# Optimization experiments

Hardware: AMD Instinct MI355X
Metric: run time of the kernel (lower is better)

The kernel has to match this reference:

```python
import jax, jax.numpy as jnp
import numpy as np

N_NODES = 50000
N_EDGES = 800000
EPS = 0.1

def setup_inputs() -> dict:
    key = jax.random.key(0)
    ks = jax.random.split(key, 6)
    x = jax.random.normal(ks[0], (N_NODES, 256), dtype=jnp.float32)
    edge_index = jax.random.randint(ks[1], (2, N_EDGES), 0, N_NODES, dtype=jnp.int64)
    W1 = jax.random.normal(ks[2], (256, 64), dtype=jnp.float32) * (1.0 / np.sqrt(256))
    b1 = jnp.zeros((64,), dtype=jnp.float32)
    att = jax.random.normal(ks[3], (2, 1, 64), dtype=jnp.float32) * (1.0 / np.sqrt(64))
    W2 = jax.random.normal(ks[4], (64, 16), dtype=jnp.float32) * (1.0 / np.sqrt(64))
    b2 = jnp.zeros((16,), dtype=jnp.float32)
    return {"x": x, "edge_index": edge_index, "W1": W1, "b1": b1, "att": att, "W2": W2, "b2": b2}

def _fagcn_conv(x, row, col, norm, att_l, eps):
    # message: norm * x_j gathered at source (row), scatter-add to target (col)
    msg = norm[:, None] * x[row]                      # [E_tot, H]
    x_l = jax.ops.segment_sum(msg, col, num_segments=N_NODES)  # low-pass
    x_h = -eps * x_l                                   # high-pass message = -eps * low message
    gate = jax.nn.sigmoid(jnp.sum(x * att_l, axis=-1, keepdims=True))  # [N,1]
    return gate * x_l + (1.0 - gate) * x_h

def reference(x, edge_index, W1, b1, att, W2, b2):
    # add self loops once (same edge set is reused by every layer)
    loops = jnp.arange(N_NODES, dtype=edge_index.dtype)
    row = jnp.concatenate([edge_index[0], loops])
    col = jnp.concatenate([edge_index[1], loops])
    deg = jax.ops.segment_sum(jnp.ones_like(col, dtype=x.dtype), col, num_segments=N_NODES)
    dinv = jnp.where(deg > 0, jax.lax.rsqrt(jnp.maximum(deg, 1e-30)), 0.0)
    norm = dinv[row] * dinv[col]                       # [E_tot]
    # eval mode: dropout is identity
    h = jax.nn.relu(x @ W1 + b1)                       # [N, H]
    for l in range(att.shape[0]):
        h = _fagcn_conv(h, row, col, norm, att[l], EPS)
    return h @ W2 + b2                                 # [N, out]
```

## Files before the change

### kernel.cpp

```cpp
#include <hip/hip_runtime.h>
#include <math.h>

#define N_FEAT_IN 256
#define N_HID 64
#define N_OUT 16
#define EPS 0.1f

typedef short bf16x8 __attribute__((ext_vector_type(8)));
typedef float f32x4 __attribute__((ext_vector_type(4)));

__device__ inline uint pack2(ushort a, ushort b) { return (uint)a | ((uint)b << 16); }

__device__ inline ushort bf16_rne(float x) {
    uint b = __float_as_uint(x);
    b += 0x7fff + ((b >> 16) & 1);
    return (ushort)(b >> 16);
}

__device__ inline float blo(uint u) { return __uint_as_float(u << 16); }
__device__ inline float bhi(uint u) { return __uint_as_float(u & 0xffff0000u); }

__device__ inline void split_bf16(float x, ushort& hi, ushort& lo) {
    uint b = __float_as_uint(x);
    hi = (ushort)(b >> 16);
    float xl = x - __uint_as_float(b & 0xffff0000u);
    lo = (ushort)(__float_as_uint(xl) >> 16);
}


__global__ void zero_int(int* __restrict__ p, int n) {
    int i = blockIdx.x * blockDim.x + threadIdx.x;
    if (i < n) p[i] = 0;
}


__global__ void hist_rank(const int* __restrict__ col, const int* __restrict__ row,
                          int* __restrict__ cnt, uint* __restrict__ rr, int E) {
    int e = blockIdx.x * blockDim.x + threadIdx.x;
    if (e < E) {
        int r = atomicAdd(&cnt[col[e]], 1);
        rr[e] = ((uint)r << 16) | (uint)row[e];
    }
}


__global__ void scan_chunks(const int* __restrict__ cnt, int* __restrict__ rowptr,
                            int* __restrict__ partial, float* __restrict__ dinv, int N) {
    __shared__ int sm[256];
    int tid = threadIdx.x;
    int gid = blockIdx.x * 256 + tid;
    int v = (gid < N) ? cnt[gid] : 0;
    sm[tid] = v;
    __syncthreads();
#pragma unroll
    for (int off = 1; off < 256; off <<= 1) {
        int add = (tid >= off) ? sm[tid - off] : 0;
        __syncthreads();
        sm[tid] += add;
        __syncthreads();
    }
    if (gid < N) {
        rowptr[gid] = sm[tid] - v;
        dinv[gid] = rsqrtf(1.0f + (float)v);
    }
    if (tid == 255) partial[blockIdx.x] = sm[255];
}


__global__ void scan_finish(int* __restrict__ rowptr, const int* __restrict__ partial,
                            int N, int E, int nchunks) {
    __shared__ int sm[256];
    int tid = threadIdx.x;
    sm[tid] = (tid < nchunks) ? partial[tid] : 0;
    __syncthreads();
#pragma unroll
    for (int off = 1; off < 256; off <<= 1) {
        int add = (tid >= off) ? sm[tid - off] : 0;
        __syncthreads();
        sm[tid] += add;
        __syncthreads();
    }
    int boff = (blockIdx.x == 0) ? 0 : sm[blockIdx.x - 1];
    __syncthreads();
    int gid = blockIdx.x * 256 + tid;
    if (gid < N) rowptr[gid] += boff;
    if (gid == 0) rowptr[N] = E;
}


__global__ void csr_scatter_part(const int* __restrict__ col, const uint* __restrict__ rr,
                                 const int* __restrict__ rowptr,
                                 ushort* __restrict__ srcidx, int E, int rangeSz) {
    int r = blockIdx.x & 7;
    int nsl = gridDim.x >> 3;
    int s = blockIdx.x >> 3;
    int lo = r * rangeSz;
    int hi = lo + rangeSz;
    int stride = nsl * blockDim.x;
    for (int e = s * blockDim.x + threadIdx.x; e < E; e += stride) {
        int c = col[e];
        if (c >= lo && c < hi) {
            uint v = rr[e];
            srcidx[rowptr[c] + (v >> 16)] = (ushort)(v & 0xffffu);
        }
    }
}


__global__ __launch_bounds__(256) void gemm1_mfma(const float* __restrict__ x,
                                                  const float* __restrict__ W1,
                                                  const float* __restrict__ b1,
                                                  const float* __restrict__ dinv,
                                                  uint* __restrict__ AsOut,
                                                  int MB) {
    __shared__ uint4 wh_lds[2048];
    __shared__ uint4 wl_lds[2048];
    __shared__ float4 xt4[1024];
    int tid = threadIdx.x;
    for (int e = tid; e < 2048; e += 256) {
        int ks = e >> 8;
        int rem = e & 255;
        int nt = rem >> 6;
        int ln = rem & 63;
        int k0 = ks * 32 + ((ln >> 4) << 3);
        int colw = nt * 16 + (ln & 15);
        ushort hi[8], lo[8];
#pragma unroll
        for (int i = 0; i < 8; ++i) {
            float v = W1[(k0 + i) * 64 + colw];
            split_bf16(v, hi[i], lo[i]);
        }
        wh_lds[e] = make_uint4(pack2(hi[0], hi[1]), pack2(hi[2], hi[3]),
                               pack2(hi[4], hi[5]), pack2(hi[6], hi[7]));
        wl_lds[e] = make_uint4(pack2(lo[0], lo[1]), pack2(lo[2], lo[3]),
                               pack2(lo[4], lo[5]), pack2(lo[6], lo[7]));
    }

    int lane = tid & 63;
    int m = lane & 15;
    int g = lane >> 4;
    int w = tid >> 6;
    const bf16x8* whf = reinterpret_cast<const bf16x8*>(wh_lds);
    const bf16x8* wlf = reinterpret_cast<const bf16x8*>(wl_lds);
    float bias = b1[w * 16 + m];
    int swz = m & 7;

    for (int mb = blockIdx.x; mb < MB; mb += gridDim.x) {
        __syncthreads();
        const float4* xg = reinterpret_cast<const float4*>(x) + (size_t)mb * 1024;
#pragma unroll
        for (int t = 0; t < 4; ++t) {
            int F = t * 256 + tid;
            int r = F >> 6, c4 = F & 63;
            xt4[r * 64 + (c4 ^ (r & 7))] = xg[F];
        }
        __syncthreads();

        f32x4 acc = {0.f, 0.f, 0.f, 0.f};
#pragma unroll
        for (int ks = 0; ks < 8; ++ks) {
            int c4 = ks * 8 + g * 2;
            float4 a0 = xt4[m * 64 + ((c4) ^ swz)];
            float4 a1 = xt4[m * 64 + ((c4 + 1) ^ swz)];
            float f[8] = {a0.x, a0.y, a0.z, a0.w, a1.x, a1.y, a1.z, a1.w};
            bf16x8 ah, al;
#pragma unroll
            for (int i = 0; i < 8; ++i) {
                ushort hu, lu;
                split_bf16(f[i], hu, lu);
                ah[i] = (short)hu;
                al[i] = (short)lu;
            }
            bf16x8 wh = whf[(ks * 4 + w) * 64 + lane];
            bf16x8 wl = wlf[(ks * 4 + w) * 64 + lane];
            acc = __builtin_amdgcn_mfma_f32_16x16x32_bf16(ah, wh, acc, 0, 0, 0);
            acc = __builtin_amdgcn_mfma_f32_16x16x32_bf16(al, wh, acc, 0, 0, 0);
            acc = __builtin_amdgcn_mfma_f32_16x16x32_bf16(ah, wl, acc, 0, 0, 0);
        }

        int r0 = mb * 16 + g * 4;
#pragma unroll
        for (int j = 0; j < 4; ++j) {
            float v = fmaxf(acc[j] + bias, 0.0f) * dinv[r0 + j];
            float p = __shfl_xor(v, 1, 64);
            if ((m & 1) == 0) {
                uint u = pack2(bf16_rne(v), bf16_rne(p));
                AsOut[(size_t)(r0 + j) * 32 + ((w * 16 + m) >> 1)] = u;
            }
        }
    }
}


template <bool LAST>
__global__ __launch_bounds__(256) void fagcn_layer(
    const uint4* __restrict__ As4, uint4* __restrict__ Out4,
    const float* __restrict__ dinv, const int* __restrict__ rowptr,
    const ushort* __restrict__ src, const float* __restrict__ att_l,
    const float* __restrict__ W2, const float* __restrict__ b2,
    float* __restrict__ out, int N) {
    __shared__ float W2s[64 * 16];
    __shared__ float hL[32 * 68];
    int tid = threadIdx.x;
    if (LAST) {
        for (int e = tid; e < 64 * 16; e += 256) W2s[e] = W2[e];
        __syncthreads();
    }
    int sub = tid & 7;
    int lnode = tid >> 3;
    int i = blockIdx.x * 32 + lnode;
    if (i >= N) i = N - 1;

    int start = rowptr[i];
    int end = rowptr[i + 1];
    const uint4* Ab = As4 + sub;
    uint4 su = Ab[(size_t)i * 8];
    float s0 = blo(su.x), s1 = bhi(su.x), s2 = blo(su.y), s3 = bhi(su.y);
    float s4 = blo(su.z), s5 = bhi(su.z), s6 = blo(su.w), s7 = bhi(su.w);

    float aA0=0.f,aA1=0.f,aA2=0.f,aA3=0.f,aA4=0.f,aA5=0.f,aA6=0.f,aA7=0.f;
    float aB0=0.f,aB1=0.f,aB2=0.f,aB3=0.f,aB4=0.f,aB5=0.f,aB6=0.f,aB7=0.f;
    int j = start;
    for (; j + 3 < end; j += 4) {
        int e0 = src[j];
        int e1 = src[j + 1];
        int e2 = src[j + 2];
        int e3 = src[j + 3];
        uint4 u0 = Ab[(size_t)e0 * 8];
        uint4 u1 = Ab[(size_t)e1 * 8];
        uint4 u2 = Ab[(size_t)e2 * 8];
        uint4 u3 = Ab[(size_t)e3 * 8];
        aA0 += blo(u0.x); aA1 += bhi(u0.x); aA2 += blo(u0.y); aA3 += bhi(u0.y);
        aA4 += blo(u0.z); aA5 += bhi(u0.z); aA6 += blo(u0.w); aA7 += bhi(u0.w);
        aB0 += blo(u1.x); aB1 += bhi(u1.x); aB2 += blo(u1.y); aB3 += bhi(u1.y);
        aB4 += blo(u1.z); aB5 += bhi(u1.z); aB6 += blo(u1.w); aB7 += bhi(u1.w);
        aA0 += blo(u2.x); aA1 += bhi(u2.x); aA2 += blo(u2.y); aA3 += bhi(u2.y);
        aA4 += blo(u2.z); aA5 += bhi(u2.z); aA6 += blo(u2.w); aA7 += bhi(u2.w);
        aB0 += blo(u3.x); aB1 += bhi(u3.x); aB2 += blo(u3.y); aB3 += bhi(u3.y);
        aB4 += blo(u3.z); aB5 += bhi(u3.z); aB6 += blo(u3.w); aB7 += bhi(u3.w);
    }
    for (; j < end; ++j) {
        int s = src[j];
        uint4 u = Ab[(size_t)s * 8];
        aA0 += blo(u.x); aA1 += bhi(u.x); aA2 += blo(u.y); aA3 += bhi(u.y);
        aA4 += blo(u.z); aA5 += bhi(u.z); aA6 += blo(u.w); aA7 += bhi(u.w);
    }
    float c0 = aA0 + aB0, c1 = aA1 + aB1, c2 = aA2 + aB2, c3 = aA3 + aB3;
    float c4 = aA4 + aB4, c5 = aA5 + aB5, c6 = aA6 + aB6, c7 = aA7 + aB7;

    float d = dinv[i];
    float4 at0 = reinterpret_cast<const float4*>(att_l)[2 * sub];
    float4 at1 = reinterpret_cast<const float4*>(att_l)[2 * sub + 1];
    float prod = s0 * at0.x + s1 * at0.y + s2 * at0.z + s3 * at0.w +
                 s4 * at1.x + s5 * at1.y + s6 * at1.z + s7 * at1.w;
#pragma unroll
    for (int off = 4; off > 0; off >>= 1)
        prod += __shfl_xor(prod, off, 64);
    float gate = 1.0f / (1.0f + expf(-prod / d));
    float factor = gate * (1.0f + EPS) - EPS;
    float df = d * factor;
    float h0 = df * (c0 + s0), h1 = df * (c1 + s1);
    float h2 = df * (c2 + s2), h3 = df * (c3 + s3);
    float h4 = df * (c4 + s4), h5 = df * (c5 + s5);
    float h6 = df * (c6 + s6), h7 = df * (c7 + s7);

    if (!LAST) {
        Out4[(size_t)i * 8 + sub] =
            make_uint4(pack2(bf16_rne(d * h0), bf16_rne(d * h1)),
                       pack2(bf16_rne(d * h2), bf16_rne(d * h3)),
                       pack2(bf16_rne(d * h4), bf16_rne(d * h5)),
                       pack2(bf16_rne(d * h6), bf16_rne(d * h7)));
    } else {
        float4* hrow4 = reinterpret_cast<float4*>(&hL[lnode * 68]);
        hrow4[2 * sub]     = make_float4(h0, h1, h2, h3);
        hrow4[2 * sub + 1] = make_float4(h4, h5, h6, h7);
        __syncthreads();
        const float4* h4p = reinterpret_cast<const float4*>(&hL[lnode * 68]);
        float accA = b2[sub];
        float accB = b2[sub + 8];
#pragma unroll
        for (int k4 = 0; k4 < 16; ++k4) {
            float4 hv = h4p[k4];
            int k = 4 * k4;
            accA = fmaf(hv.x, W2s[(k + 0) * 16 + sub], accA);
            accB = fmaf(hv.x, W2s[(k + 0) * 16 + sub + 8], accB);
            accA = fmaf(hv.y, W2s[(k + 1) * 16 + sub], accA);
            accB = fmaf(hv.y, W2s[(k + 1) * 16 + sub + 8], accB);
            accA = fmaf(hv.z, W2s[(k + 2) * 16 + sub], accA);
            accB = fmaf(hv.z, W2s[(k + 2) * 16 + sub + 8], accB);
            accA = fmaf(hv.w, W2s[(k + 3) * 16 + sub], accA);
            accB = fmaf(hv.w, W2s[(k + 3) * 16 + sub + 8], accB);
        }
        out[(size_t)i * 16 + sub] = accA;
        out[(size_t)i * 16 + sub + 8] = accB;
    }
}

extern "C" void kernel_launch(void* const* d_in, const int* in_sizes, int n_in,
                              void* d_out, int out_size, void* d_ws, size_t ws_size,
                              hipStream_t stream) {
    const float* x   = (const float*)d_in[0];
    const int*   ei  = (const int*)d_in[1];
    const float* W1  = (const float*)d_in[2];
    const float* b1  = (const float*)d_in[3];
    const float* att = (const float*)d_in[4];
    const float* W2  = (const float*)d_in[5];
    const float* b2  = (const float*)d_in[6];
    float* out = (float*)d_out;

    const int N = in_sizes[0] / N_FEAT_IN;
    const int E = in_sizes[1] / 2;
    const int L = in_sizes[4] / N_HID;

    const int* row = ei;
    const int* col = ei + E;

    char* wp = (char*)d_ws;
    auto alloc = [&](size_t bytes) -> char* {
        char* p = wp;
        wp += (bytes + 255) & ~(size_t)255;
        return p;
    };
    float*  dinv    = (float*)alloc((size_t)N * 4);
    int*    cnt     = (int*)alloc((size_t)N * 4);
    int*    rowptr  = (int*)alloc((size_t)(N + 1) * 4);
    uint*   rr      = (uint*)alloc((size_t)E * 4);
    int*    partial = (int*)alloc(256 * 4);
    ushort* srcidx  = (ushort*)alloc((size_t)E * 2);
    uint*   AsA     = (uint*)alloc((size_t)N * 32 * 4);
    uint*   AsB     = (uint*)alloc((size_t)N * 32 * 4);

    const int TB = 256;
    const int nchunks = (N + TB - 1) / TB;
    const int rangeSz = (N + 7) / 8;
    const int PART_GRID = 1024;

    zero_int<<<(N + TB - 1) / TB, TB, 0, stream>>>(cnt, N);
    hist_rank<<<(E + TB - 1) / TB, TB, 0, stream>>>(col, row, cnt, rr, E);
    scan_chunks<<<nchunks, TB, 0, stream>>>(cnt, rowptr, partial, dinv, N);
    scan_finish<<<nchunks, TB, 0, stream>>>(rowptr, partial, N, E, nchunks);
    csr_scatter_part<<<PART_GRID, TB, 0, stream>>>(col, rr, rowptr, srcidx, E, rangeSz);

    {
        const int blocks = 512;
        const int MB = N / 16;
        gemm1_mfma<<<blocks, TB, 0, stream>>>(x, W1, b1, dinv, AsA, MB);
    }

    {
        int grid = (N + 31) / 32;
        uint4* A = (uint4*)AsA;
        uint4* B = (uint4*)AsB;
        for (int l = 0; l < L; ++l) {
            const float* att_l = att + (size_t)l * N_HID;
            if (l == L - 1) {
                fagcn_layer<true><<<grid, TB, 0, stream>>>(
                    A, B, dinv, rowptr, srcidx, att_l, W2, b2, out, N);
            } else {
                fagcn_layer<false><<<grid, TB, 0, stream>>>(
                    A, B, dinv, rowptr, srcidx, att_l, W2, b2, out, N);
                uint4* tmp = A; A = B; B = tmp;
            }
        }
    }
}
```

Baseline: 123.1 us.

## Split hidden features into two half-width planes and aggregate each in separate passes

The bf16 hidden state is stored as two separate 32-feature arrays (low and high halves) instead of one 64-wide row. Each FAGCN layer runs as two kernels, each gathering only one half, so the random-access working set per pass is halved and fits better in cache. The final W2 projection moves into a standalone bf16 GEMV kernel. In exchange there are twice as many gather launches, every pass re-reads the edge list, and the last layer's output is rounded to bf16 before the projection, which adds precision loss. The layer count is now hardcoded to two.

```diff
diff --git a/kernel.cpp b/kernel.cpp
--- a/kernel.cpp
+++ b/kernel.cpp
@@ -65,7 +65,6 @@
     }
     if (tid == 255) partial[blockIdx.x] = sm[255];
 }
-
 
 __global__ void scan_finish(int* __restrict__ rowptr, const int* __restrict__ partial,
                             int N, int E, int nchunks) {
@@ -111,7 +110,8 @@
                                                   const float* __restrict__ W1,
                                                   const float* __restrict__ b1,
                                                   const float* __restrict__ dinv,
-                                                  uint* __restrict__ AsOut,
+                                                  uint* __restrict__ LoOut,
+                                                  uint* __restrict__ HiOut,
                                                   int MB) {
     __shared__ uint4 wh_lds[2048];
     __shared__ uint4 wl_lds[2048];
@@ -144,6 +144,8 @@
     const bf16x8* wlf = reinterpret_cast<const bf16x8*>(wl_lds);
     float bias = b1[w * 16 + m];
     int swz = m & 7;
+    uint* dstH = (w < 2) ? LoOut : HiOut;
+    int ci = ((w & 1) * 16 + m) >> 1;
 
     for (int mb = blockIdx.x; mb < MB; mb += gridDim.x) {
         __syncthreads();
@@ -185,38 +187,31 @@
             float p = __shfl_xor(v, 1, 64);
             if ((m & 1) == 0) {
                 uint u = pack2(bf16_rne(v), bf16_rne(p));
-                AsOut[(size_t)(r0 + j) * 32 + ((w * 16 + m) >> 1)] = u;
+                dstH[(size_t)(r0 + j) * 16 + ci] = u;
             }
         }
     }
 }
 
 
-template <bool LAST>
-__global__ __launch_bounds__(256) void fagcn_layer(
-    const uint4* __restrict__ As4, uint4* __restrict__ Out4,
+template <int HALF, bool LAST>
+__global__ __launch_bounds__(256) void fagcn_half(
+    const uint4* __restrict__ LoIn, const uint4* __restrict__ HiIn,
+    uint4* __restrict__ OutH,
     const float* __restrict__ dinv, const int* __restrict__ rowptr,
-    const ushort* __restrict__ src, const float* __restrict__ att_l,
-    const float* __restrict__ W2, const float* __restrict__ b2,
-    float* __restrict__ out, int N) {
-    __shared__ float W2s[64 * 16];
-    __shared__ float hL[32 * 68];
+    const ushort* __restrict__ src, const float* __restrict__ att_l, int N) {
     int tid = threadIdx.x;
-    if (LAST) {
-        for (int e = tid; e < 64 * 16; e += 256) W2s[e] = W2[e];
-        __syncthreads();
-    }
-    int sub = tid & 7;
-    int lnode = tid >> 3;
-    int i = blockIdx.x * 32 + lnode;
+    int sub = tid & 3;
+    int lnode = tid >> 2;
+    int i = blockIdx.x * 64 + lnode;
     if (i >= N) i = N - 1;
 
     int start = rowptr[i];
     int end = rowptr[i + 1];
-    const uint4* Ab = As4 + sub;
-    uint4 su = Ab[(size_t)i * 8];
-    float s0 = blo(su.x), s1 = bhi(su.x), s2 = blo(su.y), s3 = bhi(su.y);
-    float s4 = blo(su.z), s5 = bhi(su.z), s6 = blo(su.w), s7 = bhi(su.w);
+    const uint4* G = ((HALF == 0) ? LoIn : HiIn) + sub;
+
+    uint4 sl = LoIn[(size_t)i * 4 + sub];
+    uint4 sh = HiIn[(size_t)i * 4 + sub];
 
     float aA0=0.f,aA1=0.f,aA2=0.f,aA3=0.f,aA4=0.f,aA5=0.f,aA6=0.f,aA7=0.f;
     float aB0=0.f,aB1=0.f,aB2=0.f,aB3=0.f,aB4=0.f,aB5=0.f,aB6=0.f,aB7=0.f;
@@ -226,10 +221,10 @@
         int e1 = src[j + 1];
         int e2 = src[j + 2];
         int e3 = src[j + 3];
-        uint4 u0 = Ab[(size_t)e0 * 8];
-        uint4 u1 = Ab[(size_t)e1 * 8];
-        uint4 u2 = Ab[(size_t)e2 * 8];
-        uint4 u3 = Ab[(size_t)e3 * 8];
+        uint4 u0 = G[(size_t)e0 * 4];
+        uint4 u1 = G[(size_t)e1 * 4];
+        uint4 u2 = G[(size_t)e2 * 4];
+        uint4 u3 = G[(size_t)e3 * 4];
         aA0 += blo(u0.x); aA1 += bhi(u0.x); aA2 += blo(u0.y); aA3 += bhi(u0.y);
         aA4 += blo(u0.z); aA5 += bhi(u0.z); aA6 += blo(u0.w); aA7 += bhi(u0.w);
         aB0 += blo(u1.x); aB1 += bhi(u1.x); aB2 += blo(u1.y); aB3 += bhi(u1.y);
@@ -241,7 +236,7 @@
     }
     for (; j < end; ++j) {
         int s = src[j];
-        uint4 u = Ab[(size_t)s * 8];
+        uint4 u = G[(size_t)s * 4];
         aA0 += blo(u.x); aA1 += bhi(u.x); aA2 += blo(u.y); aA3 += bhi(u.y);
         aA4 += blo(u.z); aA5 += bhi(u.z); aA6 += blo(u.w); aA7 += bhi(u.w);
     }
@@ -249,51 +244,73 @@
     float c4 = aA4 + aB4, c5 = aA5 + aB5, c6 = aA6 + aB6, c7 = aA7 + aB7;
 
     float d = dinv[i];
-    float4 at0 = reinterpret_cast<const float4*>(att_l)[2 * sub];
-    float4 at1 = reinterpret_cast<const float4*>(att_l)[2 * sub + 1];
-    float prod = s0 * at0.x + s1 * at0.y + s2 * at0.z + s3 * at0.w +
-                 s4 * at1.x + s5 * at1.y + s6 * at1.z + s7 * at1.w;
-#pragma unroll
-    for (int off = 4; off > 0; off >>= 1)
+    const float4* at4 = reinterpret_cast<const float4*>(att_l);
+    float4 al0 = at4[2 * sub],     al1 = at4[2 * sub + 1];
+    float4 ah0 = at4[8 + 2 * sub], ah1 = at4[8 + 2 * sub + 1];
+    float prod =
+        blo(sl.x) * al0.x + bhi(sl.x) * al0.y + blo(sl.y) * al0.z + bhi(sl.y) * al0.w +
+        blo(sl.z) * al1.x + bhi(sl.z) * al1.y + blo(sl.w) * al1.z + bhi(sl.w) * al1.w +
+        blo(sh.x) * ah0.x + bhi(sh.x) * ah0.y + blo(sh.y) * ah0.z + bhi(sh.y) * ah0.w +
+        blo(sh.z) * ah1.x + bhi(sh.z) * ah1.y + blo(sh.w) * ah1.z + bhi(sh.w) * ah1.w;
+#pragma unroll
+    for (int off = 1; off < 4; off <<= 1)
         prod += __shfl_xor(prod, off, 64);
     float gate = 1.0f / (1.0f + expf(-prod / d));
     float factor = gate * (1.0f + EPS) - EPS;
     float df = d * factor;
+
+    uint4 sm = (HALF == 0) ? sl : sh;
+    float s0 = blo(sm.x), s1 = bhi(sm.x), s2 = blo(sm.y), s3 = bhi(sm.y);
+    float s4 = blo(sm.z), s5 = bhi(sm.z), s6 = blo(sm.w), s7 = bhi(sm.w);
     float h0 = df * (c0 + s0), h1 = df * (c1 + s1);
     float h2 = df * (c2 + s2), h3 = df * (c3 + s3);
     float h4 = df * (c4 + s4), h5 = df * (c5 + s5);
     float h6 = df * (c6 + s6), h7 = df * (c7 + s7);
 
-    if (!LAST) {
-        Out4[(size_t)i * 8 + sub] =
-            make_uint4(pack2(bf16_rne(d * h0), bf16_rne(d * h1)),
-                       pack2(bf16_rne(d * h2), bf16_rne(d * h3)),
-                       pack2(bf16_rne(d * h4), bf16_rne(d * h5)),
-                       pack2(bf16_rne(d * h6), bf16_rne(d * h7)));
-    } else {
-        float4* hrow4 = reinterpret_cast<float4*>(&hL[lnode * 68]);
-        hrow4[2 * sub]     = make_float4(h0, h1, h2, h3);
-        hrow4[2 * sub + 1] = make_float4(h4, h5, h6, h7);
-        __syncthreads();
-        const float4* h4p = reinterpret_cast<const float4*>(&hL[lnode * 68]);
-        float accA = b2[sub];
-        float accB = b2[sub + 8];
-#pragma unroll
-        for (int k4 = 0; k4 < 16; ++k4) {
-            float4 hv = h4p[k4];
-            int k = 4 * k4;
-            accA = fmaf(hv.x, W2s[(k + 0) * 16 + sub], accA);
-            accB = fmaf(hv.x, W2s[(k + 0) * 16 + sub + 8], accB);
-            accA = fmaf(hv.y, W2s[(k + 1) * 16 + sub], accA);
-            accB = fmaf(hv.y, W2s[(k + 1) * 16 + sub + 8], accB);
-            accA = fmaf(hv.z, W2s[(k + 2) * 16 + sub], accA);
-            accB = fmaf(hv.z, W2s[(k + 2) * 16 + sub + 8], accB);
-            accA = fmaf(hv.w, W2s[(k + 3) * 16 + sub], accA);
-            accB = fmaf(hv.w, W2s[(k + 3) * 16 + sub + 8], accB);
-        }
-        out[(size_t)i * 16 + sub] = accA;
-        out[(size_t)i * 16 + sub + 8] = accB;
-    }
+    float sc = LAST ? 1.0f : d;
+    OutH[(size_t)i * 4 + sub] =
+        make_uint4(pack2(bf16_rne(sc * h0), bf16_rne(sc * h1)),
+                   pack2(bf16_rne(sc * h2), bf16_rne(sc * h3)),
+                   pack2(bf16_rne(sc * h4), bf16_rne(sc * h5)),
+                   pack2(bf16_rne(sc * h6), bf16_rne(sc * h7)));
+}
+
+
+__global__ void gemm2_bf16(const uint4* __restrict__ hLo, const uint4* __restrict__ hHi,
+                           const float* __restrict__ W2, const float* __restrict__ b2,
+                           float* __restrict__ out, int N) {
+    int t = blockIdx.x * blockDim.x + threadIdx.x;
+    int r = t >> 4;
+    int c = t & 15;
+    if (r >= N) return;
+    float acc = b2[c];
+#pragma unroll
+    for (int q = 0; q < 4; ++q) {
+        uint4 u = hLo[(size_t)r * 4 + q];
+        int k = q * 8;
+        acc = fmaf(blo(u.x), W2[(k + 0) * 16 + c], acc);
+        acc = fmaf(bhi(u.x), W2[(k + 1) * 16 + c], acc);
+        acc = fmaf(blo(u.y), W2[(k + 2) * 16 + c], acc);
+        acc = fmaf(bhi(u.y), W2[(k + 3) * 16 + c], acc);
+        acc = fmaf(blo(u.z), W2[(k + 4) * 16 + c], acc);
+        acc = fmaf(bhi(u.z), W2[(k + 5) * 16 + c], acc);
+        acc = fmaf(blo(u.w), W2[(k + 6) * 16 + c], acc);
+        acc = fmaf(bhi(u.w), W2[(k + 7) * 16 + c], acc);
+    }
+#pragma unroll
+    for (int q = 0; q < 4; ++q) {
+        uint4 u = hHi[(size_t)r * 4 + q];
+        int k = 32 + q * 8;
+        acc = fmaf(blo(u.x), W2[(k + 0) * 16 + c], acc);
+        acc = fmaf(bhi(u.x), W2[(k + 1) * 16 + c], acc);
+        acc = fmaf(blo(u.y), W2[(k + 2) * 16 + c], acc);
+        acc = fmaf(bhi(u.y), W2[(k + 3) * 16 + c], acc);
+        acc = fmaf(blo(u.z), W2[(k + 4) * 16 + c], acc);
+        acc = fmaf(bhi(u.z), W2[(k + 5) * 16 + c], acc);
+        acc = fmaf(blo(u.w), W2[(k + 6) * 16 + c], acc);
+        acc = fmaf(bhi(u.w), W2[(k + 7) * 16 + c], acc);
+    }
+    out[(size_t)r * 16 + c] = acc;
 }
 
 extern "C" void kernel_launch(void* const* d_in, const int* in_sizes, int n_in,
@@ -310,7 +327,6 @@
 
     const int N = in_sizes[0] / N_FEAT_IN;
     const int E = in_sizes[1] / 2;
-    const int L = in_sizes[4] / N_HID;
 
     const int* row = ei;
     const int* col = ei + E;
@@ -327,8 +343,10 @@
     uint*   rr      = (uint*)alloc((size_t)E * 4);
     int*    partial = (int*)alloc(256 * 4);
     ushort* srcidx  = (ushort*)alloc((size_t)E * 2);
-    uint*   AsA     = (uint*)alloc((size_t)N * 32 * 4);
-    uint*   AsB     = (uint*)alloc((size_t)N * 32 * 4);
+    uint*   LoA     = (uint*)alloc((size_t)N * 16 * 4);
+    uint*   HiA     = (uint*)alloc((size_t)N * 16 * 4);
+    uint*   LoB     = (uint*)alloc((size_t)N * 16 * 4);
+    uint*   HiB     = (uint*)alloc((size_t)N * 16 * 4);
 
     const int TB = 256;
     const int nchunks = (N + TB - 1) / TB;
@@ -344,23 +362,22 @@
     {
         const int blocks = 512;
         const int MB = N / 16;
-        gemm1_mfma<<<blocks, TB, 0, stream>>>(x, W1, b1, dinv, AsA, MB);
+        gemm1_mfma<<<blocks, TB, 0, stream>>>(x, W1, b1, dinv, LoA, HiA, MB);
     }
 
     {
-        int grid = (N + 31) / 32;
-        uint4* A = (uint4*)AsA;
-        uint4* B = (uint4*)AsB;
-        for (int l = 0; l < L; ++l) {
-            const float* att_l = att + (size_t)l * N_HID;
-            if (l == L - 1) {
-                fagcn_layer<true><<<grid, TB, 0, stream>>>(
-                    A, B, dinv, rowptr, srcidx, att_l, W2, b2, out, N);
-            } else {
-                fagcn_layer<false><<<grid, TB, 0, stream>>>(
-                    A, B, dinv, rowptr, srcidx, att_l, W2, b2, out, N);
-                uint4* tmp = A; A = B; B = tmp;
-            }
-        }
-    }
-}
+        int grid = (N + 63) / 64;
+        const uint4* lA = (const uint4*)LoA; const uint4* hA = (const uint4*)HiA;
+        uint4* lB = (uint4*)LoB; uint4* hB = (uint4*)HiB;
+        fagcn_half<0, false><<<grid, TB, 0, stream>>>(lA, hA, lB, dinv, rowptr, srcidx, att, N);
+        fagcn_half<1, false><<<grid, TB, 0, stream>>>(lA, hA, hB, dinv, rowptr, srcidx, att, N);
+        fagcn_half<0, true><<<grid, TB, 0, stream>>>(lB, hB, (uint4*)LoA, dinv, rowptr, srcidx, att + 64, N);
+        fagcn_half<1, true><<<grid, TB, 0, stream>>>(lB, hB, (uint4*)HiA, dinv, rowptr, srcidx, att + 64, N);
+    }
+
+    {
+        long long threads = (long long)N * N_OUT;
+        gemm2_bf16<<<(int)((threads + TB - 1) / TB), TB, 0, stream>>>(
+            (const uint4*)LoA, (const uint4*)HiA, W2, b2, out, N);
+    }
+}
```

New measurement: 148.8 us, median of 2. 1.21x slower.
